# Optimization experiments

Measured on AMD Instinct MI355X. Metric: run time of the kernel, lower is better.

## Reference

```python
import jax, jax.numpy as jnp
import numpy as np

KAPPA = 0.5  # decorrelation/whitening blend


def setup_inputs() -> dict:
    B, L, D, O = 8, 4096, 1024, 2048
    NS = 1024  # int(sample_frac * L) with sample_frac = 0.25
    key = jax.random.key(0)
    k1, k2, k3, k4, k5 = jax.random.split(key, 5)
    x = jax.random.normal(k1, (B, L, D), dtype=jnp.float32)
    weight = jax.random.normal(k2, (O, D), dtype=jnp.float32) * 0.02
    bias = jax.random.normal(k3, (O,), dtype=jnp.float32) * 0.02
    # decorr matrix initialized at identity; add a small perturbation so the
    # covariance/whitening statistics are non-trivial
    decorr = jnp.eye(D, dtype=jnp.float32) + 0.01 * jax.random.normal(k4, (D, D), dtype=jnp.float32)
    sample_idx = jax.random.randint(k5, (B, NS), 0, L, dtype=jnp.int64)
    return {"x": x, "weight": weight, "bias": bias, "decorr": decorr,
            "sample_idx": sample_idx}


def reference(x, weight, bias, decorr, sample_idx):
    B, L, D = x.shape
    # fused main path: y = x @ (W @ Q)^T + b
    fused = weight @ decorr                      # (O, D)
    y = jnp.einsum('bld,od->blo', x, fused) + bias

    # --- decorrelation statistics (torch.no_grad in original) ---
    sel = jnp.take_along_axis(x, sample_idx[..., None], axis=1)   # (B, NS, D)
    sd = jnp.einsum('bnd,ed->bne', sel, decorr)                   # (B, NS, D)
    sd = sd.reshape(-1, D)                                        # (N, D)
    N = sd.shape[0]

    s2 = sd * sd                                                  # (N, D)
    norm2 = jnp.sum(s2, axis=-1)                                  # (N,) = sum_i x_i^2
    s4 = jnp.sum(s2 * s2, axis=-1)                                # (N,) = sum_i x_i^4
    inv_dd = 1.0 / (D * D)
    # C = x x^T with zeroed diagonal; mean(C^2) per sample = ((sum x^2)^2 - sum x^4)/D^2
    correlation_loss = jnp.mean(norm2 * norm2 - s4) * inv_dd
    # V = diag(x^2) - I (diagonal only); mean(V^2) per sample = sum (x_i^2-1)^2 / D^2
    whitening_loss = jnp.mean(jnp.sum((s2 - 1.0) ** 2, axis=-1)) * inv_dd

    # grad = mean_b[(1-k)*C + k*V], computed from a single GEMM X^T X
    M = (sd.T @ sd) / N                                           # (D, D) mean of xx^T
    dg = jnp.mean(s2, axis=0)                                     # (D,) mean of x^2
    Dg = jnp.diag(dg)
    I = jnp.eye(D, dtype=x.dtype)
    grad = (1.0 - KAPPA) * (M - Dg) + KAPPA * (Dg - I)

    return y, grad, correlation_loss, whitening_loss
```

## Files before the change

### kernel.cpp

```cpp
#include <hip/hip_runtime.h>
#include <hip/hip_bf16.h>
#include <cstdint>

typedef unsigned short ushortT;
typedef __attribute__((ext_vector_type(8))) short short8;
typedef __attribute__((ext_vector_type(4))) float f32x4;
typedef __attribute__((ext_vector_type(4))) unsigned short us4;

__device__ __forceinline__ ushortT f2bf(float f) {
  union { float f; unsigned u; } v; v.f = f;
  unsigned r = (v.u + 0x7FFFu + ((v.u >> 16) & 1u)) >> 16;
  return (ushortT)r;
}

__device__ __forceinline__ void gl_lds16(const void* g, void* l) {
  __builtin_amdgcn_global_load_lds(
      (__attribute__((address_space(1))) void*)g,
      (__attribute__((address_space(3))) void*)l, 16, 0, 0);
}

__global__ __launch_bounds__(512, 4) void gemm256(
    const ushortT* __restrict__ A, const ushortT* __restrict__ B,
    int M, int N, int K,
    float* __restrict__ outF, const float* __restrict__ bias)
{
  __shared__ ushortT smem[3 * 256 * 32 + 3 * 128 * 32];
  ushortT(*sA)[256 * 32] = (ushortT(*)[256 * 32])smem;
  ushortT(*sB)[128 * 32] = (ushortT(*)[128 * 32])(smem + 3 * 256 * 32);

  const int tid = threadIdx.x;
  const int wv = tid >> 6, l = tid & 63;
  const int wm = wv >> 1, wn = wv & 1;

  const int bid = blockIdx.x;
  const int xcd = bid & 7, i = bid >> 3;
  const int n0 = (i & 15) * 128;
  const int m0 = (xcd * 16 + (i >> 4)) * 256;
  const int NK = K >> 5;

  f32x4 acc[4][4] = {};

  const ushortT* Ab = A + (size_t)m0 * (size_t)K;
  const ushortT* Bb = B + (size_t)n0 * (size_t)K;

  const int sr = tid >> 2;
  const int sg = tid & 3;
  const int gsw = sg ^ ((sr >> 1) & 3);

  auto stage = [&](int kt) {
    const int b = kt % 3;
    const size_t kof = (size_t)((kt << 5) + (gsw << 3));
    gl_lds16(Ab + (size_t)sr * (size_t)K + kof,         &sA[b][(wv * 16) * 32]);
    gl_lds16(Ab + (size_t)(128 + sr) * (size_t)K + kof, &sA[b][(128 + wv * 16) * 32]);
    gl_lds16(Bb + (size_t)sr * (size_t)K + kof,         &sB[b][(wv * 16) * 32]);
  };

  const int fr = l & 15;
  const int colsw = (((l >> 4) ^ ((fr >> 1) & 3)) << 3);

  stage(0);
  stage(1);

  for (int kt = 0; kt < NK; ++kt) {
    if (kt + 1 < NK) asm volatile("s_waitcnt vmcnt(3)" ::: "memory");
    else             asm volatile("s_waitcnt vmcnt(0)" ::: "memory");
    __builtin_amdgcn_s_barrier();
    if (kt + 2 < NK) stage(kt + 2);

    const int bc = kt % 3;
    short8 av[4], bv8[4];
#pragma unroll
    for (int fi = 0; fi < 4; ++fi)
      av[fi] = *(const short8*)&sA[bc][(wm * 64 + fi * 16 + fr) * 32 + colsw];
#pragma unroll
    for (int fj = 0; fj < 4; ++fj)
      bv8[fj] = *(const short8*)&sB[bc][(wn * 64 + fj * 16 + fr) * 32 + colsw];

    __builtin_amdgcn_s_setprio(1);
#pragma unroll
    for (int fi = 0; fi < 4; ++fi)
#pragma unroll
      for (int fj = 0; fj < 4; ++fj)
        acc[fi][fj] = __builtin_amdgcn_mfma_f32_16x16x32_bf16(
            av[fi], bv8[fj], acc[fi][fj], 0, 0, 0);
    __builtin_amdgcn_s_setprio(0);
  }

  const int cc = l & 15, r4 = (l >> 4) * 4;
  float bvv[4];
#pragma unroll
  for (int fj = 0; fj < 4; ++fj) bvv[fj] = bias[n0 + wn * 64 + fj * 16 + cc];

  float* lbuf = (float*)smem;
#pragma unroll
  for (int s = 0; s < 2; ++s) {
    __syncthreads();
    if ((wm >> 1) == s) {
#pragma unroll
      for (int fi = 0; fi < 4; ++fi)
#pragma unroll
        for (int r = 0; r < 4; ++r) {
          const int row = (wm & 1) * 64 + fi * 16 + r4 + r;
#pragma unroll
          for (int fj = 0; fj < 4; ++fj)
            lbuf[row * 132 + wn * 64 + fj * 16 + cc] = acc[fi][fj][r] + bvv[fj];
        }
    }
    __syncthreads();
#pragma unroll
    for (int k = 0; k < 8; ++k) {
      const int f = k * 512 + tid;
      const int row = f >> 5, c4 = f & 31;
      f32x4 v = *(const f32x4*)&lbuf[row * 132 + c4 * 4];
      __builtin_nontemporal_store(
          v, (f32x4*)&outF[(size_t)(m0 + s * 128 + row) * (size_t)N + n0 + c4 * 4]);
    }
  }
}

template <int EPI>
__global__ __launch_bounds__(256) void gemm128(
    const ushortT* __restrict__ A, const ushortT* __restrict__ B,
    int M, int N, int K,
    float* __restrict__ outF, ushortT* __restrict__ outBF,
    const float* __restrict__ bias,
    const float* __restrict__ addend,
    float* __restrict__ S2, float* __restrict__ S4,
    ushortT* __restrict__ sdT, int ldT)
{
  __shared__ ushortT sA[2][128 * 32];
  __shared__ ushortT sB[2][128 * 32];
  const int tid = threadIdx.x;
  const int w = tid >> 6, l = tid & 63;
  const int wr = w >> 1, wc = w & 1;
  const int m0 = blockIdx.x * 128, n0 = blockIdx.y * 128;
  const int NK = K >> 5;

  f32x4 acc[4][4] = {};

  auto stage = [&](int buf, int kt) {
    const int k0 = kt << 5;
    const size_t colA = (size_t)(k0 + (l & 3) * 8);
    const int rb = w * 16 + (l >> 2);
#pragma unroll
    for (int c = 0; c < 2; ++c) {
      gl_lds16(A + (size_t)(m0 + c * 64 + rb) * (size_t)K + colA,
               &sA[buf][c * 2048 + w * 512]);
      gl_lds16(B + (size_t)(n0 + c * 64 + rb) * (size_t)K + colA,
               &sB[buf][c * 2048 + w * 512]);
    }
  };

  stage(0, 0);
  __syncthreads();

  for (int kt = 0; kt < NK; ++kt) {
    const int buf = kt & 1;
    if (kt + 1 < NK) stage(buf ^ 1, kt + 1);
    const int ro = (l & 15) * 32 + (l >> 4) * 8;
    short8 a[4], b[4];
#pragma unroll
    for (int f = 0; f < 4; ++f) {
      a[f] = *(const short8*)&sA[buf][(wr * 64 + f * 16) * 32 + ro];
      b[f] = *(const short8*)&sB[buf][(wc * 64 + f * 16) * 32 + ro];
    }
#pragma unroll
    for (int fi = 0; fi < 4; ++fi)
#pragma unroll
      for (int fj = 0; fj < 4; ++fj)
        acc[fi][fj] = __builtin_amdgcn_mfma_f32_16x16x32_bf16(
            a[fi], b[fj], acc[fi][fj], 0, 0, 0);
    __syncthreads();
  }

  const int r4 = (l >> 4) * 4, cc = l & 15;

  if constexpr (EPI == 1) {
#pragma unroll
    for (int fi = 0; fi < 4; ++fi)
#pragma unroll
      for (int r = 0; r < 4; ++r) {
        const size_t gm = (size_t)(m0 + wr * 64 + fi * 16 + r4 + r);
#pragma unroll
        for (int fj = 0; fj < 4; ++fj) {
          const int gn = n0 + wc * 64 + fj * 16 + cc;
          outBF[gm * (size_t)N + gn] = f2bf(acc[fi][fj][r]);
        }
      }
  } else {
    __shared__ ushortT tbuf[128 * 136];
#pragma unroll
    for (int fi = 0; fi < 4; ++fi)
#pragma unroll
      for (int r = 0; r < 4; ++r) {
        const int row = wr * 64 + fi * 16 + r4 + r;
        const size_t gm = (size_t)(m0 + row);
        float rs2 = 0.f, rs4 = 0.f;
#pragma unroll
        for (int fj = 0; fj < 4; ++fj) {
          const int col = wc * 64 + fj * 16 + cc;
          float sd = acc[fi][fj][r] + addend[gm * (size_t)N + n0 + col];
          tbuf[col * 136 + row] = f2bf(sd);
          float s2 = sd * sd;
          rs2 += s2;
          rs4 += s2 * s2;
        }
#pragma unroll
        for (int mk = 1; mk < 16; mk <<= 1) {
          rs2 += __shfl_xor(rs2, mk, 16);
          rs4 += __shfl_xor(rs4, mk, 16);
        }
        if (cc == 0) { atomicAdd(&S2[gm], rs2); atomicAdd(&S4[gm], rs4); }
      }
    __syncthreads();
#pragma unroll
    for (int i = 0; i < 8; ++i) {
      const int er = i * 16 + (tid >> 4);
      const int nc = (tid & 15) * 8;
      short8 v = *(const short8*)&tbuf[er * 136 + nc];
      *(short8*)&sdT[(size_t)(n0 + er) * (size_t)ldT + m0 + nc] = v;
    }
  }
}

__global__ __launch_bounds__(256) void mgemm128sk(
    const ushortT* __restrict__ T, int Dm, int K,
    float* __restrict__ pbuf)
{
  __shared__ ushortT sA[2][128 * 32];
  __shared__ ushortT sB[2][128 * 32];
  const int tid = threadIdx.x, w = tid >> 6, l = tid & 63;
  const int wr = w >> 1, wc = w & 1;
  const int i0 = blockIdx.x * 128, j0 = blockIdx.y * 128;
  const int kt0 = blockIdx.z * 64;
  f32x4 acc[4][4] = {};

  auto stage = [&](int buf, int kt) {
    const int k0 = kt << 5;
    const size_t col = (size_t)(k0 + (l & 3) * 8);
    const int rb = w * 16 + (l >> 2);
#pragma unroll
    for (int c = 0; c < 2; ++c) {
      gl_lds16(T + (size_t)(i0 + c * 64 + rb) * (size_t)K + col,
               &sA[buf][c * 2048 + w * 512]);
      gl_lds16(T + (size_t)(j0 + c * 64 + rb) * (size_t)K + col,
               &sB[buf][c * 2048 + w * 512]);
    }
  };

  stage(0, kt0);
  __syncthreads();

  for (int t = 0; t < 64; ++t) {
    const int buf = t & 1;
    if (t + 1 < 64) stage(buf ^ 1, kt0 + t + 1);
    const int ro = (l & 15) * 32 + (l >> 4) * 8;
    short8 a[4], b[4];
#pragma unroll
    for (int f = 0; f < 4; ++f) {
      a[f] = *(const short8*)&sA[buf][(wr * 64 + f * 16) * 32 + ro];
      b[f] = *(const short8*)&sB[buf][(wc * 64 + f * 16) * 32 + ro];
    }
#pragma unroll
    for (int fi = 0; fi < 4; ++fi)
#pragma unroll
      for (int fj = 0; fj < 4; ++fj)
        acc[fi][fj] = __builtin_amdgcn_mfma_f32_16x16x32_bf16(
            a[fi], b[fj], acc[fi][fj], 0, 0, 0);
    __syncthreads();
  }

  const int r4 = (l >> 4) * 4, cc = l & 15;
  float* out = pbuf + ((size_t)blockIdx.z << 20);
#pragma unroll
  for (int fi = 0; fi < 4; ++fi)
#pragma unroll
    for (int r = 0; r < 4; ++r) {
      const int gi = i0 + wr * 64 + fi * 16 + r4 + r;
#pragma unroll
      for (int fj = 0; fj < 4; ++fj) {
        const int gj = j0 + wc * 64 + fj * 16 + cc;
        out[(size_t)gi * (size_t)Dm + gj] = acc[fi][fj][r];
      }
    }
}

__global__ void reduce_grad(const float* __restrict__ pbuf,
                            float* __restrict__ grad, float invN) {
  const int i = blockIdx.x * 256 + threadIdx.x;
  const size_t base = (size_t)i * 4;
  f32x4 s = *(const f32x4*)(pbuf + base) + *(const f32x4*)(pbuf + base + (1u << 20)) +
            *(const f32x4*)(pbuf + base + (2u << 20)) + *(const f32x4*)(pbuf + base + (3u << 20));
  const int row = (int)(base >> 10), c0 = (int)(base & 1023);
  f32x4 o;
#pragma unroll
  for (int j = 0; j < 4; ++j)
    o[j] = 0.5f * (s[j] * invN) - ((row == c0 + j) ? 0.5f : 0.0f);
  *(f32x4*)(grad + base) = o;
}

__global__ void zero_f32(float* __restrict__ p, int n) {
  int i = blockIdx.x * blockDim.x + threadIdx.x;
  if (i < n) p[i] = 0.f;
}

__global__ void cvt_f32_bf16(const float* __restrict__ in, ushortT* __restrict__ out,
                             size_t n4) {
  size_t i = (size_t)blockIdx.x * blockDim.x + threadIdx.x;
  const size_t stride = (size_t)gridDim.x * blockDim.x;
  const f32x4* in4 = (const f32x4*)in;
  for (; i < n4; i += stride) {
    f32x4 v = __builtin_nontemporal_load(&in4[i]);
    us4 o = { f2bf(v.x), f2bf(v.y), f2bf(v.z), f2bf(v.w) };
    *(us4*)(out + i * 4) = o;
  }
}

__global__ __launch_bounds__(256) void transposeQ(const float* __restrict__ q,
                                                  ushortT* __restrict__ qT) {
  __shared__ float t[128][129];
  const int bi = blockIdx.x, bj = blockIdx.y;
  const int tr = threadIdx.x >> 5, tc = threadIdx.x & 31;
#pragma unroll
  for (int i = 0; i < 16; ++i) {
    const int row = i * 8 + tr;
    f32x4 v = *(const f32x4*)&q[(size_t)(bi * 128 + row) * 1024 + bj * 128 + tc * 4];
#pragma unroll
    for (int j = 0; j < 4; ++j) t[row][tc * 4 + j] = v[j];
  }
  __syncthreads();
#pragma unroll
  for (int i = 0; i < 16; ++i) {
    const int dr = i * 8 + tr;
    us4 o = { f2bf(t[tc * 4 + 0][dr]), f2bf(t[tc * 4 + 1][dr]),
              f2bf(t[tc * 4 + 2][dr]), f2bf(t[tc * 4 + 3][dr]) };
    *(us4*)&qT[(size_t)(bj * 128 + dr) * 1024 + bi * 128 + tc * 4] = o;
  }
}

__global__ void make_p(const float* __restrict__ q, ushortT* __restrict__ p) {
  const int g = blockIdx.x * 256 + threadIdx.x;
  const size_t base = (size_t)g * 8;
  const int e = (int)(base >> 10);
  const int d0 = (int)(base & 1023);
  short8 v;
#pragma unroll
  for (int j = 0; j < 8; ++j) {
    float f = q[base + j] - ((e == d0 + j) ? 1.0f : 0.0f);
    v[j] = (short)f2bf(f);
  }
  *(short8*)(p + base) = v;
}

__global__ void gather_rows(const float* __restrict__ x, const int* __restrict__ idx,
                            float* __restrict__ self32, ushortT* __restrict__ selbf) {
  const int bid = blockIdx.x;
  const int b = bid >> 10;
  const int row = idx[bid] & 4095;
  const float4* src = (const float4*)(x + ((size_t)b * 4096 + (size_t)row) * 1024);
  const int t = threadIdx.x;
  float4 v = src[t];
  *(float4*)(self32 + (size_t)bid * 1024 + t * 4) = v;
  us4 o = { f2bf(v.x), f2bf(v.y), f2bf(v.z), f2bf(v.w) };
  *(us4*)(selbf + (size_t)bid * 1024 + t * 4) = o;
}

__global__ void loss_final(const float* __restrict__ S2, const float* __restrict__ S4,
                           float* __restrict__ out) {
  __shared__ double red0[256];
  __shared__ double red1[256];
  const int t = threadIdx.x;
  double ca = 0.0, wa = 0.0;
  for (int i = t; i < 8192; i += 256) {
    double s2 = (double)S2[i], s4 = (double)S4[i];
    ca += s2 * s2 - s4;
    wa += s4 - 2.0 * s2 + 1024.0;
  }
  red0[t] = ca; red1[t] = wa;
  __syncthreads();
  for (int s = 128; s > 0; s >>= 1) {
    if (t < s) { red0[t] += red0[t + s]; red1[t] += red1[t + s]; }
    __syncthreads();
  }
  if (t == 0) {
    const double inv = 1.0 / (8192.0 * 1024.0 * 1024.0);
    out[0] = (float)(red0[0] * inv);
    out[1] = (float)(red1[0] * inv);
  }
}

extern "C" void kernel_launch(void* const* d_in, const int* in_sizes, int n_in,
                              void* d_out, int out_size, void* d_ws, size_t ws_size,
                              hipStream_t stream) {
  (void)in_sizes; (void)n_in; (void)out_size;
  const float* x = (const float*)d_in[0];
  const float* weight = (const float*)d_in[1];
  const float* bias = (const float*)d_in[2];
  const float* decorr = (const float*)d_in[3];
  const int* sidx = (const int*)d_in[4];

  if (ws_size < 146866176ULL) return;

  char* ws = (char*)d_ws;
  ushortT* xbf     = (ushortT*)(ws);
  ushortT* fusedbf = (ushortT*)(ws + 67108864);
  ushortT* wbf     = (ushortT*)(ws + 71303168);
  ushortT* qT      = (ushortT*)(ws + 75497472);
  ushortT* pbf     = (ushortT*)(ws + 77594624);
  float*   self32  = (float*)  (ws + 79691776);
  ushortT* selbf   = (ushortT*)(ws + 113246208);
  ushortT* sdT     = (ushortT*)(ws + 130023424);
  float*   S2      = (float*)  (ws + 146800640);
  float*   S4      = (float*)  (ws + 146833408);

  float* y = (float*)d_out;
  float* grad = y + 67108864ULL;
  float* losses = grad + 1048576ULL;

  zero_f32<<<dim3(64), dim3(256), 0, stream>>>(S2, 16384);
  cvt_f32_bf16<<<dim3(2048), dim3(256), 0, stream>>>(x, xbf, 8388608);
  cvt_f32_bf16<<<dim3(512), dim3(256), 0, stream>>>(weight, wbf, 524288);
  transposeQ<<<dim3(8, 8), dim3(256), 0, stream>>>(decorr, qT);
  make_p<<<dim3(512), dim3(256), 0, stream>>>(decorr, pbf);
  gather_rows<<<dim3(8192), dim3(256), 0, stream>>>(x, sidx, self32, selbf);

  gemm128<1><<<dim3(16, 8), dim3(256), 0, stream>>>(
      wbf, qT, 2048, 1024, 1024, nullptr, fusedbf, nullptr, nullptr,
      nullptr, nullptr, nullptr, 0);
  gemm256<<<dim3(2048), dim3(512), 0, stream>>>(
      xbf, fusedbf, 32768, 2048, 1024, y, bias);
  gemm128<2><<<dim3(64, 8), dim3(256), 0, stream>>>(
      selbf, pbf, 8192, 1024, 1024, nullptr, nullptr, nullptr, self32,
      S2, S4, sdT, 8192);
  mgemm128sk<<<dim3(8, 8, 4), dim3(256), 0, stream>>>(sdT, 1024, 8192, self32);
  reduce_grad<<<dim3(1024), dim3(256), 0, stream>>>(self32, grad, 1.0f / 8192.0f);
  loss_final<<<dim3(1), dim3(256), 0, stream>>>(S2, S4, losses);
}
```

Measured before the change: 326.3 us.

## Enlarge main GEMM tile to 256x256 with 4-stage split A/B pipeline

Replaces the 256x128-tile main GEMM with a 256x256 tile per 512-thread block, using 4 LDS stages (128 KB) and a ping-pong schedule. Each k-step issues its global loads in two halves (A then B) interleaved with two MFMA phases over the upper and lower row halves. This is meant to improve data reuse per block, halve the block count and overlap loads with compute more finely. In exchange, LDS use and accumulator registers double, occupancy drops to about 2 blocks per CU, and the epilogue now writes output in four 64-row passes.

```diff
diff --git a/kernel.cpp b/kernel.cpp
--- a/kernel.cpp
+++ b/kernel.cpp
@@ -19,26 +19,23 @@
       (__attribute__((address_space(3))) void*)l, 16, 0, 0);
 }
 
-__global__ __launch_bounds__(512, 4) void gemm256(
+__global__ __launch_bounds__(512, 2) void gemm8p(
     const ushortT* __restrict__ A, const ushortT* __restrict__ B,
     int M, int N, int K,
     float* __restrict__ outF, const float* __restrict__ bias)
 {
-  __shared__ ushortT smem[3 * 256 * 32 + 3 * 128 * 32];
-  ushortT(*sA)[256 * 32] = (ushortT(*)[256 * 32])smem;
-  ushortT(*sB)[128 * 32] = (ushortT(*)[128 * 32])(smem + 3 * 256 * 32);
-
+  __shared__ ushortT smem[4 * 2 * 256 * 32];
   const int tid = threadIdx.x;
   const int wv = tid >> 6, l = tid & 63;
-  const int wm = wv >> 1, wn = wv & 1;
+  const int wm = wv >> 2, wn = wv & 3;
 
   const int bid = blockIdx.x;
-  const int xcd = bid & 7, i = bid >> 3;
-  const int n0 = (i & 15) * 128;
-  const int m0 = (xcd * 16 + (i >> 4)) * 256;
+  const int xcd = bid & 7, ii = bid >> 3;
+  const int n0 = (ii & 7) * 256;
+  const int m0 = (xcd * 16 + (ii >> 3)) * 256;
   const int NK = K >> 5;
 
-  f32x4 acc[4][4] = {};
+  f32x4 acc[8][4] = {};
 
   const ushortT* Ab = A + (size_t)m0 * (size_t)K;
   const ushortT* Bb = B + (size_t)n0 * (size_t)K;
@@ -47,43 +44,68 @@
   const int sg = tid & 3;
   const int gsw = sg ^ ((sr >> 1) & 3);
 
-  auto stage = [&](int kt) {
-    const int b = kt % 3;
-    const size_t kof = (size_t)((kt << 5) + (gsw << 3));
-    gl_lds16(Ab + (size_t)sr * (size_t)K + kof,         &sA[b][(wv * 16) * 32]);
-    gl_lds16(Ab + (size_t)(128 + sr) * (size_t)K + kof, &sA[b][(128 + wv * 16) * 32]);
-    gl_lds16(Bb + (size_t)sr * (size_t)K + kof,         &sB[b][(wv * 16) * 32]);
+  auto stageA = [&](int kt, int half) {
+    ushortT* base = smem + (kt & 3) * 16384;
+    const int r = half * 128 + sr;
+    gl_lds16(Ab + (size_t)r * (size_t)K + (size_t)((kt << 5) + (gsw << 3)),
+             base + (half * 128 + (wv << 4)) * 32);
+  };
+  auto stageB = [&](int kt, int half) {
+    ushortT* base = smem + (kt & 3) * 16384 + 8192;
+    const int r = half * 128 + sr;
+    gl_lds16(Bb + (size_t)r * (size_t)K + (size_t)((kt << 5) + (gsw << 3)),
+             base + (half * 128 + (wv << 4)) * 32);
   };
 
   const int fr = l & 15;
   const int colsw = (((l >> 4) ^ ((fr >> 1) & 3)) << 3);
 
-  stage(0);
-  stage(1);
+  for (int t = 0; t < 3; ++t) { stageA(t, 0); stageA(t, 1); stageB(t, 0); stageB(t, 1); }
+  asm volatile("s_waitcnt vmcnt(8)" ::: "memory");
+  __builtin_amdgcn_s_barrier();
 
   for (int kt = 0; kt < NK; ++kt) {
-    if (kt + 1 < NK) asm volatile("s_waitcnt vmcnt(3)" ::: "memory");
-    else             asm volatile("s_waitcnt vmcnt(0)" ::: "memory");
+    const ushortT* sAb = smem + (kt & 3) * 16384;
+    const ushortT* sBb = sAb + 8192;
+    short8 a[4], b[4];
+
+    if (kt + 3 < NK) { stageA(kt + 3, 0); stageA(kt + 3, 1); }
+#pragma unroll
+    for (int fi = 0; fi < 4; ++fi)
+      a[fi] = *(const short8*)&sAb[(wm * 128 + fi * 16 + fr) * 32 + colsw];
+#pragma unroll
+    for (int fj = 0; fj < 4; ++fj)
+      b[fj] = *(const short8*)&sBb[(wn * 64 + fj * 16 + fr) * 32 + colsw];
     __builtin_amdgcn_s_barrier();
-    if (kt + 2 < NK) stage(kt + 2);
-
-    const int bc = kt % 3;
-    short8 av[4], bv8[4];
-#pragma unroll
-    for (int fi = 0; fi < 4; ++fi)
-      av[fi] = *(const short8*)&sA[bc][(wm * 64 + fi * 16 + fr) * 32 + colsw];
-#pragma unroll
-    for (int fj = 0; fj < 4; ++fj)
-      bv8[fj] = *(const short8*)&sB[bc][(wn * 64 + fj * 16 + fr) * 32 + colsw];
-
     __builtin_amdgcn_s_setprio(1);
 #pragma unroll
     for (int fi = 0; fi < 4; ++fi)
 #pragma unroll
       for (int fj = 0; fj < 4; ++fj)
         acc[fi][fj] = __builtin_amdgcn_mfma_f32_16x16x32_bf16(
-            av[fi], bv8[fj], acc[fi][fj], 0, 0, 0);
+            a[fi], b[fj], acc[fi][fj], 0, 0, 0);
     __builtin_amdgcn_s_setprio(0);
+    __builtin_amdgcn_s_barrier();
+
+    if (kt + 3 < NK) { stageB(kt + 3, 0); stageB(kt + 3, 1); }
+#pragma unroll
+    for (int fi = 0; fi < 4; ++fi)
+      a[fi] = *(const short8*)&sAb[(wm * 128 + 64 + fi * 16 + fr) * 32 + colsw];
+    if (kt + 1 < NK) {
+      if (kt + 3 < NK)      asm volatile("s_waitcnt vmcnt(8)" ::: "memory");
+      else if (kt + 2 < NK) asm volatile("s_waitcnt vmcnt(4)" ::: "memory");
+      else                  asm volatile("s_waitcnt vmcnt(0)" ::: "memory");
+    }
+    __builtin_amdgcn_s_barrier();
+    __builtin_amdgcn_s_setprio(1);
+#pragma unroll
+    for (int fi = 0; fi < 4; ++fi)
+#pragma unroll
+      for (int fj = 0; fj < 4; ++fj)
+        acc[4 + fi][fj] = __builtin_amdgcn_mfma_f32_16x16x32_bf16(
+            a[fi], b[fj], acc[4 + fi][fj], 0, 0, 0);
+    __builtin_amdgcn_s_setprio(0);
+    __builtin_amdgcn_s_barrier();
   }
 
   const int cc = l & 15, r4 = (l >> 4) * 4;
@@ -93,27 +115,28 @@
 
   float* lbuf = (float*)smem;
 #pragma unroll
-  for (int s = 0; s < 2; ++s) {
-    __syncthreads();
-    if ((wm >> 1) == s) {
-#pragma unroll
-      for (int fi = 0; fi < 4; ++fi)
+  for (int s = 0; s < 4; ++s) {
+    __syncthreads();
+    if (wm == (s >> 1)) {
+#pragma unroll
+      for (int fi2 = 0; fi2 < 4; ++fi2)
 #pragma unroll
         for (int r = 0; r < 4; ++r) {
-          const int row = (wm & 1) * 64 + fi * 16 + r4 + r;
+          const int fi = (s & 1) * 4 + fi2;
+          const int row = fi2 * 16 + r4 + r;
 #pragma unroll
           for (int fj = 0; fj < 4; ++fj)
-            lbuf[row * 132 + wn * 64 + fj * 16 + cc] = acc[fi][fj][r] + bvv[fj];
+            lbuf[row * 260 + wn * 64 + fj * 16 + cc] = acc[fi][fj][r] + bvv[fj];
         }
     }
     __syncthreads();
 #pragma unroll
-    for (int k = 0; k < 8; ++k) {
-      const int f = k * 512 + tid;
-      const int row = f >> 5, c4 = f & 31;
-      f32x4 v = *(const f32x4*)&lbuf[row * 132 + c4 * 4];
+    for (int k2 = 0; k2 < 8; ++k2) {
+      const int f = k2 * 512 + tid;
+      const int row = f >> 6, c4 = f & 63;
+      f32x4 v = *(const f32x4*)&lbuf[row * 260 + c4 * 4];
       __builtin_nontemporal_store(
-          v, (f32x4*)&outF[(size_t)(m0 + s * 128 + row) * (size_t)N + n0 + c4 * 4]);
+          v, (f32x4*)&outF[(size_t)(m0 + s * 64 + row) * (size_t)N + n0 + c4 * 4]);
     }
   }
 }
@@ -427,7 +450,7 @@
   gemm128<1><<<dim3(16, 8), dim3(256), 0, stream>>>(
       wbf, qT, 2048, 1024, 1024, nullptr, fusedbf, nullptr, nullptr,
       nullptr, nullptr, nullptr, 0);
-  gemm256<<<dim3(2048), dim3(512), 0, stream>>>(
+  gemm8p<<<dim3(1024), dim3(512), 0, stream>>>(
       xbf, fusedbf, 32768, 2048, 1024, y, bias);
   gemm128<2><<<dim3(64, 8), dim3(256), 0, stream>>>(
       selbf, pbf, 8192, 1024, 1024, nullptr, nullptr, nullptr, self32,
```

Measured after the change: 331.2 us. No clear change (+1.5%).

## Fuse x fp32-to-bf16 conversion into main GEMM A-load and merge prep kernels

Applied to the files above, without the earlier changes.

The main GEMM now reads fp32 x directly into registers, converts it with packed bf16 conversion instructions and writes it to LDS, replacing a separate full-size conversion pass over x and its bf16 round trip through memory. The small preparation kernels (weight conversion, decorr transpose, P construction, S2/S4 zeroing) are merged into one launch. In exchange, each GEMM tile rereads x at fp32 width for every N-tile, doubling A-side global traffic, and the A path moves from direct global-to-LDS loads to register staging with an extra LDS wait.

```diff
diff --git a/kernel.cpp b/kernel.cpp
--- a/kernel.cpp
+++ b/kernel.cpp
@@ -13,17 +13,24 @@
   return (ushortT)r;
 }
 
+__device__ __forceinline__ unsigned cvtpk(float lo, float hi) {
+  unsigned r;
+  asm("v_cvt_pk_bf16_f32 %0, %1, %2" : "=v"(r) : "v"(lo), "v"(hi));
+  return r;
+}
+
 __device__ __forceinline__ void gl_lds16(const void* g, void* l) {
   __builtin_amdgcn_global_load_lds(
       (__attribute__((address_space(1))) void*)g,
       (__attribute__((address_space(3))) void*)l, 16, 0, 0);
 }
 
-__global__ __launch_bounds__(512, 4) void gemm256(
-    const ushortT* __restrict__ A, const ushortT* __restrict__ B,
-    int M, int N, int K,
+__global__ __launch_bounds__(512, 4) void gemmfx(
+    const float* __restrict__ X, const ushortT* __restrict__ B,
     float* __restrict__ outF, const float* __restrict__ bias)
 {
+  constexpr int NK = 32;
+  constexpr int N = 2048;
   __shared__ ushortT smem[3 * 256 * 32 + 3 * 128 * 32];
   ushortT(*sA)[256 * 32] = (ushortT(*)[256 * 32])smem;
   ushortT(*sB)[128 * 32] = (ushortT(*)[128 * 32])(smem + 3 * 256 * 32);
@@ -33,57 +40,87 @@
   const int wm = wv >> 1, wn = wv & 1;
 
   const int bid = blockIdx.x;
-  const int xcd = bid & 7, i = bid >> 3;
-  const int n0 = (i & 15) * 128;
-  const int m0 = (xcd * 16 + (i >> 4)) * 256;
-  const int NK = K >> 5;
+  const int xcd = bid & 7, ii = bid >> 3;
+  const int n0 = (ii & 15) * 128;
+  const int m0 = (xcd * 16 + (ii >> 4)) * 256;
 
   f32x4 acc[4][4] = {};
 
-  const ushortT* Ab = A + (size_t)m0 * (size_t)K;
-  const ushortT* Bb = B + (size_t)n0 * (size_t)K;
-
-  const int sr = tid >> 2;
-  const int sg = tid & 3;
-  const int gsw = sg ^ ((sr >> 1) & 3);
-
-  auto stage = [&](int kt) {
-    const int b = kt % 3;
-    const size_t kof = (size_t)((kt << 5) + (gsw << 3));
-    gl_lds16(Ab + (size_t)sr * (size_t)K + kof,         &sA[b][(wv * 16) * 32]);
-    gl_lds16(Ab + (size_t)(128 + sr) * (size_t)K + kof, &sA[b][(128 + wv * 16) * 32]);
-    gl_lds16(Bb + (size_t)sr * (size_t)K + kof,         &sB[b][(wv * 16) * 32]);
+  const int ar = tid >> 1;
+  const int ak = (tid & 1) * 16;
+  const int aswz = (ar >> 1) & 3;
+  const int ga0 = (tid & 1) * 2, ga1 = ga0 + 1;
+  const float* Xrow = X + (size_t)(m0 + ar) * 1024 + ak;
+
+  const ushortT* Bb = B + (size_t)n0 * 1024;
+  const int rb = tid >> 2;
+  const int gsb = (tid & 3) ^ ((rb >> 1) & 3);
+  auto stageB = [&](int kt) {
+    gl_lds16(Bb + (size_t)rb * 1024 + (size_t)((kt << 5) + (gsb << 3)),
+             &sB[kt % 3][(wv * 16) * 32]);
+  };
+
+  auto writeA = [&](int kt, f32x4 (&wr)[4]) {
+    ushortT* dst = &sA[kt % 3][ar * 32];
+    union { unsigned u[4]; short8 s; } p0, p1;
+    p0.u[0] = cvtpk(wr[0][0], wr[0][1]); p0.u[1] = cvtpk(wr[0][2], wr[0][3]);
+    p0.u[2] = cvtpk(wr[1][0], wr[1][1]); p0.u[3] = cvtpk(wr[1][2], wr[1][3]);
+    p1.u[0] = cvtpk(wr[2][0], wr[2][1]); p1.u[1] = cvtpk(wr[2][2], wr[2][3]);
+    p1.u[2] = cvtpk(wr[3][0], wr[3][1]); p1.u[3] = cvtpk(wr[3][2], wr[3][3]);
+    *(short8*)&dst[(ga0 ^ aswz) << 3] = p0.s;
+    *(short8*)&dst[(ga1 ^ aswz) << 3] = p1.s;
   };
 
   const int fr = l & 15;
   const int colsw = (((l >> 4) ^ ((fr >> 1) & 3)) << 3);
 
-  stage(0);
-  stage(1);
-
-  for (int kt = 0; kt < NK; ++kt) {
-    if (kt + 1 < NK) asm volatile("s_waitcnt vmcnt(3)" ::: "memory");
-    else             asm volatile("s_waitcnt vmcnt(0)" ::: "memory");
+  f32x4 ra0[4], ra1[4];
+
+#pragma unroll
+  for (int j = 0; j < 4; ++j) ra0[j] = *(const f32x4*)(Xrow + j * 4);
+  stageB(0);
+#pragma unroll
+  for (int j = 0; j < 4; ++j) ra1[j] = *(const f32x4*)(Xrow + 32 + j * 4);
+  stageB(1);
+  asm volatile("s_waitcnt vmcnt(5)" ::: "memory");
+  writeA(0, ra0);
+
+  auto body = [&](int kt, f32x4 (&wr)[4], f32x4 (&ld)[4]) {
+    if (kt + 2 < NK) {
+#pragma unroll
+      for (int j = 0; j < 4; ++j)
+        ld[j] = *(const f32x4*)(Xrow + (kt + 2) * 32 + j * 4);
+      asm volatile("s_waitcnt vmcnt(4)" ::: "memory");
+    } else {
+      asm volatile("s_waitcnt vmcnt(0)" ::: "memory");
+    }
+    if (kt + 1 < NK) writeA(kt + 1, wr);
+    asm volatile("s_waitcnt lgkmcnt(0)" ::: "memory");
     __builtin_amdgcn_s_barrier();
-    if (kt + 2 < NK) stage(kt + 2);
-
-    const int bc = kt % 3;
-    short8 av[4], bv8[4];
-#pragma unroll
-    for (int fi = 0; fi < 4; ++fi)
-      av[fi] = *(const short8*)&sA[bc][(wm * 64 + fi * 16 + fr) * 32 + colsw];
-#pragma unroll
-    for (int fj = 0; fj < 4; ++fj)
-      bv8[fj] = *(const short8*)&sB[bc][(wn * 64 + fj * 16 + fr) * 32 + colsw];
-
+    if (kt + 2 < NK) stageB(kt + 2);
+
+    const ushortT* cA = sA[kt % 3];
+    const ushortT* cB = sB[kt % 3];
+    short8 av[4], bv[4];
+#pragma unroll
+    for (int f = 0; f < 4; ++f) {
+      av[f] = *(const short8*)&cA[(wm * 64 + f * 16 + fr) * 32 + colsw];
+      bv[f] = *(const short8*)&cB[(wn * 64 + f * 16 + fr) * 32 + colsw];
+    }
     __builtin_amdgcn_s_setprio(1);
 #pragma unroll
     for (int fi = 0; fi < 4; ++fi)
 #pragma unroll
       for (int fj = 0; fj < 4; ++fj)
         acc[fi][fj] = __builtin_amdgcn_mfma_f32_16x16x32_bf16(
-            av[fi], bv8[fj], acc[fi][fj], 0, 0, 0);
+            av[fi], bv[fj], acc[fi][fj], 0, 0, 0);
     __builtin_amdgcn_s_setprio(0);
+  };
+
+#pragma unroll 1
+  for (int kt2 = 0; kt2 < NK; kt2 += 2) {
+    body(kt2, ra1, ra0);
+    body(kt2 + 1, ra0, ra1);
   }
 
   const int cc = l & 15, r4 = (l >> 4) * 4;
@@ -299,57 +336,53 @@
   *(f32x4*)(grad + base) = o;
 }
 
-__global__ void zero_f32(float* __restrict__ p, int n) {
-  int i = blockIdx.x * blockDim.x + threadIdx.x;
-  if (i < n) p[i] = 0.f;
-}
-
-__global__ void cvt_f32_bf16(const float* __restrict__ in, ushortT* __restrict__ out,
-                             size_t n4) {
-  size_t i = (size_t)blockIdx.x * blockDim.x + threadIdx.x;
-  const size_t stride = (size_t)gridDim.x * blockDim.x;
-  const f32x4* in4 = (const f32x4*)in;
-  for (; i < n4; i += stride) {
-    f32x4 v = __builtin_nontemporal_load(&in4[i]);
-    us4 o = { f2bf(v.x), f2bf(v.y), f2bf(v.z), f2bf(v.w) };
-    *(us4*)(out + i * 4) = o;
-  }
-}
-
-__global__ __launch_bounds__(256) void transposeQ(const float* __restrict__ q,
-                                                  ushortT* __restrict__ qT) {
+__global__ __launch_bounds__(256) void prep_misc(
+    const float* __restrict__ weight, const float* __restrict__ decorr,
+    ushortT* __restrict__ wbf, ushortT* __restrict__ qT,
+    ushortT* __restrict__ pbf, float* __restrict__ S2S4)
+{
   __shared__ float t[128][129];
-  const int bi = blockIdx.x, bj = blockIdx.y;
-  const int tr = threadIdx.x >> 5, tc = threadIdx.x & 31;
-#pragma unroll
-  for (int i = 0; i < 16; ++i) {
-    const int row = i * 8 + tr;
-    f32x4 v = *(const f32x4*)&q[(size_t)(bi * 128 + row) * 1024 + bj * 128 + tc * 4];
-#pragma unroll
-    for (int j = 0; j < 4; ++j) t[row][tc * 4 + j] = v[j];
-  }
-  __syncthreads();
-#pragma unroll
-  for (int i = 0; i < 16; ++i) {
-    const int dr = i * 8 + tr;
-    us4 o = { f2bf(t[tc * 4 + 0][dr]), f2bf(t[tc * 4 + 1][dr]),
-              f2bf(t[tc * 4 + 2][dr]), f2bf(t[tc * 4 + 3][dr]) };
-    *(us4*)&qT[(size_t)(bj * 128 + dr) * 1024 + bi * 128 + tc * 4] = o;
-  }
-}
-
-__global__ void make_p(const float* __restrict__ q, ushortT* __restrict__ p) {
-  const int g = blockIdx.x * 256 + threadIdx.x;
-  const size_t base = (size_t)g * 8;
-  const int e = (int)(base >> 10);
-  const int d0 = (int)(base & 1023);
-  short8 v;
-#pragma unroll
-  for (int j = 0; j < 8; ++j) {
-    float f = q[base + j] - ((e == d0 + j) ? 1.0f : 0.0f);
-    v[j] = (short)f2bf(f);
-  }
-  *(short8*)(p + base) = v;
+  const int bid = blockIdx.x;
+  const int tix = threadIdx.x;
+  if (bid < 512) {
+    const f32x4* in4 = (const f32x4*)weight;
+    for (size_t i = (size_t)bid * 256 + tix; i < 524288; i += 512 * 256) {
+      f32x4 v = in4[i];
+      us4 o = { f2bf(v[0]), f2bf(v[1]), f2bf(v[2]), f2bf(v[3]) };
+      *(us4*)(wbf + i * 4) = o;
+    }
+  } else if (bid < 1024) {
+    const size_t base = ((size_t)(bid - 512) * 256 + tix) * 8;
+    const int e = (int)(base >> 10);
+    const int d0 = (int)(base & 1023);
+    short8 v;
+#pragma unroll
+    for (int j = 0; j < 8; ++j) {
+      float f = decorr[base + j] - ((e == d0 + j) ? 1.0f : 0.0f);
+      v[j] = (short)f2bf(f);
+    }
+    *(short8*)(pbf + base) = v;
+  } else if (bid < 1088) {
+    const int bi = (bid - 1024) & 7, bj = (bid - 1024) >> 3;
+    const int tr = tix >> 5, tc = tix & 31;
+#pragma unroll
+    for (int i = 0; i < 16; ++i) {
+      const int row = i * 8 + tr;
+      f32x4 v = *(const f32x4*)&decorr[(size_t)(bi * 128 + row) * 1024 + bj * 128 + tc * 4];
+#pragma unroll
+      for (int j = 0; j < 4; ++j) t[row][tc * 4 + j] = v[j];
+    }
+    __syncthreads();
+#pragma unroll
+    for (int i = 0; i < 16; ++i) {
+      const int dr = i * 8 + tr;
+      us4 o = { f2bf(t[tc * 4 + 0][dr]), f2bf(t[tc * 4 + 1][dr]),
+                f2bf(t[tc * 4 + 2][dr]), f2bf(t[tc * 4 + 3][dr]) };
+      *(us4*)&qT[(size_t)(bj * 128 + dr) * 1024 + bi * 128 + tc * 4] = o;
+    }
+  } else {
+    S2S4[(bid - 1088) * 256 + tix] = 0.f;
+  }
 }
 
 __global__ void gather_rows(const float* __restrict__ x, const int* __restrict__ idx,
@@ -402,7 +435,6 @@
   if (ws_size < 146866176ULL) return;
 
   char* ws = (char*)d_ws;
-  ushortT* xbf     = (ushortT*)(ws);
   ushortT* fusedbf = (ushortT*)(ws + 67108864);
   ushortT* wbf     = (ushortT*)(ws + 71303168);
   ushortT* qT      = (ushortT*)(ws + 75497472);
@@ -417,18 +449,13 @@
   float* grad = y + 67108864ULL;
   float* losses = grad + 1048576ULL;
 
-  zero_f32<<<dim3(64), dim3(256), 0, stream>>>(S2, 16384);
-  cvt_f32_bf16<<<dim3(2048), dim3(256), 0, stream>>>(x, xbf, 8388608);
-  cvt_f32_bf16<<<dim3(512), dim3(256), 0, stream>>>(weight, wbf, 524288);
-  transposeQ<<<dim3(8, 8), dim3(256), 0, stream>>>(decorr, qT);
-  make_p<<<dim3(512), dim3(256), 0, stream>>>(decorr, pbf);
+  prep_misc<<<dim3(1152), dim3(256), 0, stream>>>(weight, decorr, wbf, qT, pbf, S2);
   gather_rows<<<dim3(8192), dim3(256), 0, stream>>>(x, sidx, self32, selbf);
 
   gemm128<1><<<dim3(16, 8), dim3(256), 0, stream>>>(
       wbf, qT, 2048, 1024, 1024, nullptr, fusedbf, nullptr, nullptr,
       nullptr, nullptr, nullptr, 0);
-  gemm256<<<dim3(2048), dim3(512), 0, stream>>>(
-      xbf, fusedbf, 32768, 2048, 1024, y, bias);
+  gemmfx<<<dim3(2048), dim3(512), 0, stream>>>(x, fusedbf, y, bias);
   gemm128<2><<<dim3(64, 8), dim3(256), 0, stream>>>(
       selbf, pbf, 8192, 1024, 1024, nullptr, nullptr, nullptr, self32,
       S2, S4, sdT, 8192);
```

Result: slower. 492.6 us (+51.0%).
